# Optimization experiments

Hardware: AMD Instinct MI355X
Metric: run time of the kernel (lower is better)

## Reference

```python
import jax, jax.numpy as jnp
import numpy as np


def setup_inputs() -> dict:
    key = jax.random.key(0)
    k1, k2 = jax.random.split(key)
    bs, seq, hidden = 128, 4096, 128
    decoder_state_t = jax.random.normal(k1, (bs, hidden), dtype=jnp.float32)
    encoder_states = jax.random.normal(k2, (bs, seq, hidden), dtype=jnp.float32)
    return {"decoder_state_t": decoder_state_t, "encoder_states": encoder_states}


def reference(decoder_state_t, encoder_states):
    # score[b,s] = sum_h dec[b,h] * enc[b,s,h]  (batched matvec, avoids tile)
    score = jnp.einsum('bh,bsh->bs', decoder_state_t, encoder_states)
    attn_prob = jax.nn.softmax(score, axis=-1)
    # context[b,h] = sum_s attn_prob[b,s] * enc[b,s,h]
    context = jnp.einsum('bs,bsh->bh', attn_prob, encoder_states)
    return (attn_prob, context)
```

## Files before the change

### kernel.cpp

```cpp
#include <hip/hip_runtime.h>
#include <math.h>

#define B_ 128
#define S_ 4096
#define H_ 128
#define SPLITS_ 16
#define CHUNK_ (S_ / SPLITS_)
#define NPART_ (H_ + 2)

__global__ __launch_bounds__(256) void s2s_attn_pass1(
    const float* __restrict__ dec, const float* __restrict__ enc,
    float* __restrict__ score_out, float* __restrict__ part_out) {
  const int blk = blockIdx.x;
  const int b = blk / SPLITS_;
  const int split = blk - b * SPLITS_;
  const int t = threadIdx.x;
  const int w = t >> 6;
  const int lane = t & 63;
  const int half = lane >> 5;
  const int l32 = lane & 31;

  __shared__ float s_score[CHUNK_];
  __shared__ float s_m[4];
  __shared__ float s_l[4];
  __shared__ float s_ctx[4][H_];

  const float4 dv = *reinterpret_cast<const float4*>(dec + b * H_ + l32 * 4);
  const float* encb = enc + (size_t)b * S_ * H_ + (size_t)split * CHUNK_ * H_;

  float m = -INFINITY, l = 0.f;
  float cx = 0.f, cy = 0.f, cz = 0.f, cw = 0.f;

#pragma unroll
  for (int i = 0; i < CHUNK_ / 32; ++i) {
    const int base = i * 32 + w * 8;
    const float4 e0 = *reinterpret_cast<const float4*>(
        encb + (size_t)(base + 0 + half) * H_ + l32 * 4);
    const float4 e1 = *reinterpret_cast<const float4*>(
        encb + (size_t)(base + 2 + half) * H_ + l32 * 4);
    const float4 e2 = *reinterpret_cast<const float4*>(
        encb + (size_t)(base + 4 + half) * H_ + l32 * 4);
    const float4 e3 = *reinterpret_cast<const float4*>(
        encb + (size_t)(base + 6 + half) * H_ + l32 * 4);

    float p0 = e0.x * dv.x + e0.y * dv.y + e0.z * dv.z + e0.w * dv.w;
    float p1 = e1.x * dv.x + e1.y * dv.y + e1.z * dv.z + e1.w * dv.w;
    float p2 = e2.x * dv.x + e2.y * dv.y + e2.z * dv.z + e2.w * dv.w;
    float p3 = e3.x * dv.x + e3.y * dv.y + e3.z * dv.z + e3.w * dv.w;
#pragma unroll
    for (int s = 1; s <= 16; s <<= 1) {
      p0 += __shfl_xor(p0, s);
      p1 += __shfl_xor(p1, s);
      p2 += __shfl_xor(p2, s);
      p3 += __shfl_xor(p3, s);
    }
    if (l32 == 0) {
      s_score[base + 0 + half] = p0;
      s_score[base + 2 + half] = p1;
      s_score[base + 4 + half] = p2;
      s_score[base + 6 + half] = p3;
    }
    const float mb = fmaxf(fmaxf(p0, p1), fmaxf(p2, p3));
    const float mn = fmaxf(m, mb);
    const float corr = __expf(m - mn);
    const float w0 = __expf(p0 - mn);
    const float w1 = __expf(p1 - mn);
    const float w2 = __expf(p2 - mn);
    const float w3 = __expf(p3 - mn);
    l = l * corr + (w0 + w1 + w2 + w3);
    cx = cx * corr + w0 * e0.x + w1 * e1.x + w2 * e2.x + w3 * e3.x;
    cy = cy * corr + w0 * e0.y + w1 * e1.y + w2 * e2.y + w3 * e3.y;
    cz = cz * corr + w0 * e0.z + w1 * e1.z + w2 * e2.z + w3 * e3.z;
    cw = cw * corr + w0 * e0.w + w1 * e1.w + w2 * e2.w + w3 * e3.w;
    m = mn;
  }

  const float m_o = __shfl_xor(m, 32);
  const float l_o = __shfl_xor(l, 32);
  const float cx_o = __shfl_xor(cx, 32);
  const float cy_o = __shfl_xor(cy, 32);
  const float cz_o = __shfl_xor(cz, 32);
  const float cw_o = __shfl_xor(cw, 32);
  const float M = fmaxf(m, m_o);
  const float ea = __expf(m - M);
  const float eb = __expf(m_o - M);
  if (lane == 0) { s_m[w] = M; s_l[w] = l * ea + l_o * eb; }
  if (half == 0) {
    s_ctx[w][l32 * 4 + 0] = cx * ea + cx_o * eb;
    s_ctx[w][l32 * 4 + 1] = cy * ea + cy_o * eb;
    s_ctx[w][l32 * 4 + 2] = cz * ea + cz_o * eb;
    s_ctx[w][l32 * 4 + 3] = cw * ea + cw_o * eb;
  }
  __syncthreads();

  float* part = part_out + (size_t)blk * NPART_;
  if (t < H_) {
    const float m0 = s_m[0], m1 = s_m[1], m2 = s_m[2], m3 = s_m[3];
    const float Mb = fmaxf(fmaxf(m0, m1), fmaxf(m2, m3));
    const float e0 = __expf(m0 - Mb), e1 = __expf(m1 - Mb);
    const float e2 = __expf(m2 - Mb), e3 = __expf(m3 - Mb);
    if (t == 0) {
      part[0] = Mb;
      part[1] = s_l[0] * e0 + s_l[1] * e1 + s_l[2] * e2 + s_l[3] * e3;
    }
    part[2 + t] = s_ctx[0][t] * e0 + s_ctx[1][t] * e1 +
                  s_ctx[2][t] * e2 + s_ctx[3][t] * e3;
  }

  float* so = score_out + (size_t)b * S_ + (size_t)split * CHUNK_;
  if (t < CHUNK_) so[t] = s_score[t];
}

__global__ __launch_bounds__(256) void s2s_attn_pass2(
    float* __restrict__ attn, float* __restrict__ ctx_out,
    const float* __restrict__ part_in) {
  const int b = blockIdx.x;
  const int t = threadIdx.x;
  const float* base = part_in + (size_t)b * SPLITS_ * NPART_;

  float mv[SPLITS_], lv[SPLITS_], ex[SPLITS_];
  float M = -INFINITY;
#pragma unroll
  for (int p = 0; p < SPLITS_; ++p) {
    mv[p] = base[p * NPART_];
    lv[p] = base[p * NPART_ + 1];
    M = fmaxf(M, mv[p]);
  }
  float L = 0.f;
#pragma unroll
  for (int p = 0; p < SPLITS_; ++p) {
    ex[p] = __expf(mv[p] - M);
    L += lv[p] * ex[p];
  }
  const float invL = 1.0f / L;

  if (t < H_) {
    float c = 0.f;
#pragma unroll
    for (int p = 0; p < SPLITS_; ++p) c += base[p * NPART_ + 2 + t] * ex[p];
    ctx_out[(size_t)b * H_ + t] = c * invL;
  }

  float* ab = attn + (size_t)b * S_;
#pragma unroll 4
  for (int j = t; j < S_; j += 256) ab[j] = __expf(ab[j] - M) * invL;
}

extern "C" void kernel_launch(void* const* d_in, const int* in_sizes, int n_in,
                              void* d_out, int out_size, void* d_ws, size_t ws_size,
                              hipStream_t stream) {
  const float* dec = (const float*)d_in[0];
  const float* enc = (const float*)d_in[1];
  float* out = (float*)d_out;
  float* attn = out;
  float* ctx = out + (size_t)B_ * S_;
  float* part = (float*)d_ws;

  s2s_attn_pass1<<<dim3(B_ * SPLITS_), dim3(256), 0, stream>>>(dec, enc, attn, part);
  s2s_attn_pass2<<<dim3(B_), dim3(256), 0, stream>>>(attn, ctx, part);
}
```

Before: 360.6 us.

## Fuse split-softmax passes via last-block atomic counter and nontemporal encoder loads

Merges the two kernels into one: each split block publishes its partial max/sum/context, then bumps a per-batch atomic counter, and the last block to finish does the final merge and normalizes the attention row. Encoder loads become nontemporal, and the normalization loop is vectorized to float4. This removes a kernel launch and the gap between the two passes, at the cost of a memset launch and a serialized tail done by one block per batch.

```diff
diff --git a/kernel.cpp b/kernel.cpp
--- a/kernel.cpp
+++ b/kernel.cpp
@@ -7,10 +7,14 @@
 #define SPLITS_ 16
 #define CHUNK_ (S_ / SPLITS_)
 #define NPART_ (H_ + 2)
+#define PART_OFF_ 1024
 
-__global__ __launch_bounds__(256) void s2s_attn_pass1(
+typedef float f4v __attribute__((ext_vector_type(4)));
+
+__global__ __launch_bounds__(256) void s2s_attn_fused(
     const float* __restrict__ dec, const float* __restrict__ enc,
-    float* __restrict__ score_out, float* __restrict__ part_out) {
+    float* __restrict__ attn, float* __restrict__ ctx_out,
+    float* __restrict__ part_out, int* __restrict__ counters) {
   const int blk = blockIdx.x;
   const int b = blk / SPLITS_;
   const int split = blk - b * SPLITS_;
@@ -24,8 +28,9 @@
   __shared__ float s_m[4];
   __shared__ float s_l[4];
   __shared__ float s_ctx[4][H_];
+  __shared__ int s_last;
 
-  const float4 dv = *reinterpret_cast<const float4*>(dec + b * H_ + l32 * 4);
+  const f4v dv = *reinterpret_cast<const f4v*>(dec + b * H_ + l32 * 4);
   const float* encb = enc + (size_t)b * S_ * H_ + (size_t)split * CHUNK_ * H_;
 
   float m = -INFINITY, l = 0.f;
@@ -34,14 +39,14 @@
 #pragma unroll
   for (int i = 0; i < CHUNK_ / 32; ++i) {
     const int base = i * 32 + w * 8;
-    const float4 e0 = *reinterpret_cast<const float4*>(
-        encb + (size_t)(base + 0 + half) * H_ + l32 * 4);
-    const float4 e1 = *reinterpret_cast<const float4*>(
-        encb + (size_t)(base + 2 + half) * H_ + l32 * 4);
-    const float4 e2 = *reinterpret_cast<const float4*>(
-        encb + (size_t)(base + 4 + half) * H_ + l32 * 4);
-    const float4 e3 = *reinterpret_cast<const float4*>(
-        encb + (size_t)(base + 6 + half) * H_ + l32 * 4);
+    const f4v e0 = __builtin_nontemporal_load(
+        reinterpret_cast<const f4v*>(encb + (size_t)(base + 0 + half) * H_ + l32 * 4));
+    const f4v e1 = __builtin_nontemporal_load(
+        reinterpret_cast<const f4v*>(encb + (size_t)(base + 2 + half) * H_ + l32 * 4));
+    const f4v e2 = __builtin_nontemporal_load(
+        reinterpret_cast<const f4v*>(encb + (size_t)(base + 4 + half) * H_ + l32 * 4));
+    const f4v e3 = __builtin_nontemporal_load(
+        reinterpret_cast<const f4v*>(encb + (size_t)(base + 6 + half) * H_ + l32 * 4));
 
     float p0 = e0.x * dv.x + e0.y * dv.y + e0.z * dv.z + e0.w * dv.w;
     float p1 = e1.x * dv.x + e1.y * dv.y + e1.z * dv.z + e1.w * dv.w;
@@ -107,29 +112,32 @@
                   s_ctx[2][t] * e2 + s_ctx[3][t] * e3;
   }
 
-  float* so = score_out + (size_t)b * S_ + (size_t)split * CHUNK_;
+  float* so = attn + (size_t)b * S_ + (size_t)split * CHUNK_;
   if (t < CHUNK_) so[t] = s_score[t];
-}
 
-__global__ __launch_bounds__(256) void s2s_attn_pass2(
-    float* __restrict__ attn, float* __restrict__ ctx_out,
-    const float* __restrict__ part_in) {
-  const int b = blockIdx.x;
-  const int t = threadIdx.x;
-  const float* base = part_in + (size_t)b * SPLITS_ * NPART_;
+  __threadfence();
+  __syncthreads();
+  if (t == 0) {
+    const int old = atomicAdd(&counters[b], 1);
+    s_last = (old == SPLITS_ - 1) ? 1 : 0;
+  }
+  __syncthreads();
+  if (!s_last) return;
+  __threadfence();
 
+  const float* pb = part_out + (size_t)b * SPLITS_ * NPART_;
   float mv[SPLITS_], lv[SPLITS_], ex[SPLITS_];
-  float M = -INFINITY;
+  float Mg = -INFINITY;
 #pragma unroll
   for (int p = 0; p < SPLITS_; ++p) {
-    mv[p] = base[p * NPART_];
-    lv[p] = base[p * NPART_ + 1];
-    M = fmaxf(M, mv[p]);
+    mv[p] = pb[p * NPART_];
+    lv[p] = pb[p * NPART_ + 1];
+    Mg = fmaxf(Mg, mv[p]);
   }
   float L = 0.f;
 #pragma unroll
   for (int p = 0; p < SPLITS_; ++p) {
-    ex[p] = __expf(mv[p] - M);
+    ex[p] = __expf(mv[p] - Mg);
     L += lv[p] * ex[p];
   }
   const float invL = 1.0f / L;
@@ -137,13 +145,20 @@
   if (t < H_) {
     float c = 0.f;
 #pragma unroll
-    for (int p = 0; p < SPLITS_; ++p) c += base[p * NPART_ + 2 + t] * ex[p];
+    for (int p = 0; p < SPLITS_; ++p) c += pb[p * NPART_ + 2 + t] * ex[p];
     ctx_out[(size_t)b * H_ + t] = c * invL;
   }
 
-  float* ab = attn + (size_t)b * S_;
-#pragma unroll 4
-  for (int j = t; j < S_; j += 256) ab[j] = __expf(ab[j] - M) * invL;
+  f4v* ab = reinterpret_cast<f4v*>(attn + (size_t)b * S_);
+#pragma unroll
+  for (int j = t; j < S_ / 4; j += 256) {
+    f4v v = ab[j];
+    v.x = __expf(v.x - Mg) * invL;
+    v.y = __expf(v.y - Mg) * invL;
+    v.z = __expf(v.z - Mg) * invL;
+    v.w = __expf(v.w - Mg) * invL;
+    ab[j] = v;
+  }
 }
 
 extern "C" void kernel_launch(void* const* d_in, const int* in_sizes, int n_in,
@@ -154,8 +169,10 @@
   float* out = (float*)d_out;
   float* attn = out;
   float* ctx = out + (size_t)B_ * S_;
-  float* part = (float*)d_ws;
+  int* counters = (int*)d_ws;
+  float* part = (float*)d_ws + PART_OFF_;
 
-  s2s_attn_pass1<<<dim3(B_ * SPLITS_), dim3(256), 0, stream>>>(dec, enc, attn, part);
-  s2s_attn_pass2<<<dim3(B_), dim3(256), 0, stream>>>(attn, ctx, part);
+  (void)hipMemsetAsync(counters, 0, B_ * sizeof(int), stream);
+  s2s_attn_fused<<<dim3(B_ * SPLITS_), dim3(256), 0, stream>>>(
+      dec, enc, attn, ctx, part, counters);
 }
```

After: 783.2 us. +117.2%, slower.
